# Kernel optimization log

Hardware: AMD Instinct MI355X
Metric: run time of the kernel (lower is better)

Reference implementation:

```python
import jax, jax.numpy as jnp
import numpy as np


def setup_inputs() -> dict:
    key = jax.random.key(0)
    k1, k2, k3, k4, k5 = jax.random.split(key, 5)
    B, S, H, F, E = 2, 512, 1024, 3584, 8
    scale_in = 1.0 / np.sqrt(H)
    scale_ff = 1.0 / np.sqrt(F)
    return {
        "hidden_states": jax.random.normal(k1, (B, S, H), dtype=jnp.float32),
        "gate_w": jax.random.normal(k2, (E, H), dtype=jnp.float32) * scale_in,
        "w1": jax.random.normal(k3, (E, F, H), dtype=jnp.float32) * scale_in,
        "w2": jax.random.normal(k4, (E, H, F), dtype=jnp.float32) * scale_ff,
        "w3": jax.random.normal(k5, (E, F, H), dtype=jnp.float32) * scale_in,
    }


TOP_K = 2


def reference(hidden_states, gate_w, w1, w2, w3):
    B, S, H = hidden_states.shape
    E = gate_w.shape[0]
    x = hidden_states.reshape(B * S, H)  # [T, H]
    T = x.shape[0]

    # Router: softmax in fp32, top-2 selection, renormalize selected weights.
    router_logits = x @ gate_w.T  # [T, E]
    probs = jax.nn.softmax(router_logits.astype(jnp.float32), axis=-1)
    top_vals, top_idx = jax.lax.top_k(probs, TOP_K)  # [T, K]
    top_vals = top_vals / jnp.sum(top_vals, axis=-1, keepdims=True)
    top_vals = top_vals.astype(x.dtype)

    # Dense routing-weight matrix [T, E]: weight if selected else 0
    # (equivalent to the one-hot expert_mask + index_add combine).
    dense_w = jnp.zeros((T, E), dtype=x.dtype).at[
        jnp.arange(T)[:, None], top_idx
    ].add(top_vals)

    # Expert SwiGLU MLPs, batched over the expert axis.
    h1 = jnp.einsum("th,efh->etf", x, w1)  # [E, T, F]
    h3 = jnp.einsum("th,efh->etf", x, w3)  # [E, T, F]
    y = jnp.einsum("etf,ehf->eth", jax.nn.silu(h1) * h3, w2)  # [E, T, H]

    # Weighted combine across experts.
    out = jnp.einsum("eth,te->th", y, dense_w)  # [T, H]
    return out.reshape(B, S, H), router_logits
```

## Files before the change

### kernel.cpp

```cpp
#include <hip/hip_runtime.h>
#include <hip/hip_bf16.h>

typedef __bf16 v8bf __attribute__((ext_vector_type(8)));
typedef __bf16 v4bf __attribute__((ext_vector_type(4)));
typedef float  f32x4 __attribute__((ext_vector_type(4)));
typedef unsigned int u32;

#define NTOK 1024
#define HDIM 1024
#define FDIM 3584
#define NEXP 8
#define NPAIR 2048
#define MAXT1 32
#define MAXT2 48
#define KSPLIT2 2
#define KPER2 (FDIM / KSPLIT2)

#define OFF_COUNTS   0
#define OFF_OFFSETS  64
#define OFF_NT1      128
#define OFF_NT2      132
#define OFF_T1E      192
#define OFF_T1M      320
#define OFF_T2E      448
#define OFF_T2M      640
#define OFF_TOKIDX   2048
#define OFF_TOKWT    (2048 + 4*NPAIR)
#define OFF_PAIRTOK  (OFF_TOKWT + 4*NPAIR)
#define OFF_PAIRWT   (OFF_PAIRTOK + 4*NPAIR)
#define OFF_SLOTOF   (OFF_PAIRWT + 4*NPAIR)
#define OFF_XB       65536
#define OFF_ACT      (OFF_XB + 2ull*NTOK*HDIM)
#define OFF_Y0       (OFF_ACT + 2ull*NPAIR*FDIM)
#define OFF_Y1       (OFF_Y0 + 4ull*NPAIR*HDIM)

static __device__ inline v4bf cvt4(float4 f) {
    v4bf r;
    r[0] = (__bf16)f.x; r[1] = (__bf16)f.y; r[2] = (__bf16)f.z; r[3] = (__bf16)f.w;
    return r;
}

static __device__ inline v8bf pack8(f32x4 lo, f32x4 hi) {
    v8bf r;
    r[0] = (__bf16)lo[0]; r[1] = (__bf16)lo[1]; r[2] = (__bf16)lo[2]; r[3] = (__bf16)lo[3];
    r[4] = (__bf16)hi[0]; r[5] = (__bf16)hi[1]; r[6] = (__bf16)hi[2]; r[7] = (__bf16)hi[3];
    return r;
}

#define FENCE() asm volatile("" ::: "memory")
#define BARRIER() do { FENCE(); __builtin_amdgcn_s_barrier(); FENCE(); } while (0)
#define WAITVM0() asm volatile("s_waitcnt vmcnt(0)" ::: "memory")
#define WAITLGKM0() asm volatile("s_waitcnt lgkmcnt(0)" ::: "memory")

#define DMA16(SRC, DST) \
    __builtin_amdgcn_global_load_lds((const __attribute__((address_space(1))) u32*)(SRC), \
                                     (__attribute__((address_space(3))) u32*)(DST), 16, 0, 0)

__global__ __launch_bounds__(256) void moe_cvtx(const float* __restrict__ x,
                                                __bf16* __restrict__ xb)
{
    const size_t i = ((size_t)blockIdx.x * 256 + threadIdx.x) * 4;
    float4 v = *(const float4*)(x + i);
    *(v4bf*)(xb + i) = cvt4(v);
}

__global__ __launch_bounds__(256) void moe_router(
    const float* __restrict__ x, const float* __restrict__ gw,
    float* __restrict__ logits, int* __restrict__ counts,
    int* __restrict__ tok_idx, float* __restrict__ tok_wt)
{
    const int lane = threadIdx.x & 63;
    const int wv = threadIdx.x >> 6;
    const int t = blockIdx.x * 4 + wv;
    const float* xr = x + (size_t)t * HDIM;

    float acc[NEXP];
#pragma unroll
    for (int e = 0; e < NEXP; ++e) acc[e] = 0.f;
#pragma unroll
    for (int j = 0; j < 4; ++j) {
        int h = lane * 4 + j * 256;
        float4 xv = *(const float4*)(xr + h);
#pragma unroll
        for (int e = 0; e < NEXP; ++e) {
            float4 g = *(const float4*)(gw + e * HDIM + h);
            acc[e] += xv.x * g.x + xv.y * g.y + xv.z * g.z + xv.w * g.w;
        }
    }
#pragma unroll
    for (int e = 0; e < NEXP; ++e) {
#pragma unroll
        for (int s = 32; s > 0; s >>= 1) acc[e] += __shfl_xor(acc[e], s);
    }
    if (lane == 0) {
#pragma unroll
        for (int e = 0; e < NEXP; ++e) logits[t * NEXP + e] = acc[e];
        int i0 = 0;
#pragma unroll
        for (int e = 1; e < NEXP; ++e) if (acc[e] > acc[i0]) i0 = e;
        int i1 = (i0 == 0) ? 1 : 0;
#pragma unroll
        for (int e = 0; e < NEXP; ++e) if (e != i0 && acc[e] > acc[i1]) i1 = e;
        float w0 = 1.f / (1.f + expf(acc[i1] - acc[i0]));
        float w1 = 1.f - w0;
        tok_idx[2 * t] = i0; tok_idx[2 * t + 1] = i1;
        tok_wt[2 * t] = w0;  tok_wt[2 * t + 1] = w1;
        atomicAdd(&counts[i0], 1);
        atomicAdd(&counts[i1], 1);
    }
}

__global__ void moe_scatter(const int* __restrict__ counts, const int* __restrict__ tok_idx,
                            const float* __restrict__ tok_wt, int* __restrict__ offsets,
                            int* __restrict__ pair_token, float* __restrict__ pair_wt,
                            int* __restrict__ slot_of,
                            int* __restrict__ t1e, int* __restrict__ t1m, int* __restrict__ nt1,
                            int* __restrict__ t2e, int* __restrict__ t2m, int* __restrict__ nt2)
{
    __shared__ int cur[NEXP];
    const int tid = threadIdx.x;
    if (tid == 0) {
        int run = 0, n1 = 0, n2 = 0;
        for (int e = 0; e < NEXP; ++e) {
            offsets[e] = run; cur[e] = run;
            for (int m0 = 0; m0 < counts[e]; m0 += 128) { t1e[n1] = e; t1m[n1] = m0; ++n1; }
            for (int m0 = 0; m0 < counts[e]; m0 += 64)  { t2e[n2] = e; t2m[n2] = m0; ++n2; }
            run += counts[e];
        }
        *nt1 = n1; *nt2 = n2;
    }
    __syncthreads();
    for (int p = tid; p < 2 * NTOK; p += blockDim.x) {
        int e = tok_idx[p];
        int s = atomicAdd(&cur[e], 1);
        pair_token[s] = p >> 1;
        pair_wt[s] = tok_wt[p];
        slot_of[p] = s;
    }
}

__global__ __launch_bounds__(256, 2) void moe_gemm1(
    const __bf16* __restrict__ xb, const float* __restrict__ w1g,
    const float* __restrict__ w3g, const int* __restrict__ counts,
    const int* __restrict__ offsets, const int* __restrict__ pair_token,
    const int* __restrict__ t1e, const int* __restrict__ t1m,
    const int* __restrict__ nt1,
    __bf16* __restrict__ act)
{
    const int ty = blockIdx.y;
    if (ty >= *nt1) return;
    const int e = t1e[ty];
    const int m0 = t1m[ty];
    const int Me = counts[e];
    const int rows = min(128, Me - m0);
    const int slot0 = offsets[e] + m0;
    const int n0 = blockIdx.x * 64;

    __shared__ __align__(16) __bf16 As[128 * 64];
    __shared__ __align__(16) float  B1s[64 * 64];
    __shared__ __align__(16) float  B3s[64 * 64];

    const int tid = threadIdx.x;
    const int lane = tid & 63;
    const int wv = tid >> 6;
    const int ln4 = lane >> 4;
    const int lr = lane & 15;
    const int wm = (wv >> 1) * 64;
    const int wn = (wv & 1) * 32;

    f32x4 acc1[4][2], acc3[4][2];
#pragma unroll
    for (int i = 0; i < 4; ++i)
#pragma unroll
        for (int j = 0; j < 2; ++j) {
            acc1[i][j] = (f32x4){0.f, 0.f, 0.f, 0.f};
            acc3[i][j] = (f32x4){0.f, 0.f, 0.f, 0.f};
        }

    const char* asrc[4];
#pragma unroll
    for (int i = 0; i < 4; ++i) {
        int c = i * 256 + tid;
        int r = c >> 3;
        int rr = (r < rows) ? r : 0;
        int sj = (c & 7) ^ (r & 7);
        asrc[i] = (const char*)(xb + (size_t)pair_token[slot0 + rr] * HDIM) + sj * 16;
    }
    const char* bsrc[4];
#pragma unroll
    for (int i = 0; i < 4; ++i) {
        int c = i * 256 + tid;
        int r = c >> 4;
        int sj = (c & 15) ^ (r & 15);
        bsrc[i] = (const char*)(w1g + ((size_t)e * FDIM + n0 + r) * HDIM) + sj * 16;
    }
    const ptrdiff_t d31b = (const char*)w3g - (const char*)w1g;

#define DMA_ALL1(K0) do { _Pragma("unroll") \
    for (int i = 0; i < 4; ++i) { \
        DMA16(asrc[i] + (size_t)(K0) * 128, (char*)As + (i * 256 + wv * 64) * 16); \
        DMA16(bsrc[i] + (size_t)(K0) * 256, (char*)B1s + (i * 256 + wv * 64) * 16); \
        DMA16(bsrc[i] + d31b + (size_t)(K0) * 256, (char*)B3s + (i * 256 + wv * 64) * 16); \
    } } while (0)

    int abase[4], axor[4];
#pragma unroll
    for (int i = 0; i < 4; ++i) {
        int row = wm + i * 16 + lr;
        abase[i] = row * 128;
        axor[i] = (row & 7) << 4;
    }
    int bbase[2], bxor[2];
#pragma unroll
    for (int i = 0; i < 2; ++i) {
        int row = wn + i * 16 + lr;
        bbase[i] = row * 256;
        bxor[i] = (row & 15) << 4;
    }

#define CMP1() do { \
    v8bf af[4][2]; v8bf b1f[2][2], b3f[2][2]; \
    _Pragma("unroll") \
    for (int mi = 0; mi < 4; ++mi) { _Pragma("unroll") \
        for (int ks = 0; ks < 2; ++ks) \
            af[mi][ks] = *(const v8bf*)((const char*)As + abase[mi] + ((ks * 64 + ln4 * 16) ^ axor[mi])); } \
    _Pragma("unroll") \
    for (int ni = 0; ni < 2; ++ni) { _Pragma("unroll") \
        for (int ks = 0; ks < 2; ++ks) { \
            int in0 = ks * 128 + ln4 * 32; \
            f32x4 lo1 = *(const f32x4*)((const char*)B1s + bbase[ni] + ((in0) ^ bxor[ni])); \
            f32x4 hi1 = *(const f32x4*)((const char*)B1s + bbase[ni] + ((in0 + 16) ^ bxor[ni])); \
            f32x4 lo3 = *(const f32x4*)((const char*)B3s + bbase[ni] + ((in0) ^ bxor[ni])); \
            f32x4 hi3 = *(const f32x4*)((const char*)B3s + bbase[ni] + ((in0 + 16) ^ bxor[ni])); \
            b1f[ni][ks] = pack8(lo1, hi1); \
            b3f[ni][ks] = pack8(lo3, hi3); } } \
    _Pragma("unroll") \
    for (int mi = 0; mi < 4; ++mi) { _Pragma("unroll") \
        for (int ni = 0; ni < 2; ++ni) { _Pragma("unroll") \
            for (int ks = 0; ks < 2; ++ks) { \
                acc1[mi][ni] = __builtin_amdgcn_mfma_f32_16x16x32_bf16(af[mi][ks], b1f[ni][ks], acc1[mi][ni], 0, 0, 0); \
                acc3[mi][ni] = __builtin_amdgcn_mfma_f32_16x16x32_bf16(af[mi][ks], b3f[ni][ks], acc3[mi][ni], 0, 0, 0); } } } \
    } while (0)

    DMA_ALL1(0);
    for (int ks = 0; ks < HDIM / 64; ++ks) {
        WAITVM0();
        BARRIER();
        CMP1();
        WAITLGKM0();
        BARRIER();
        if (ks + 1 < HDIM / 64) DMA_ALL1(ks + 1);
    }
#undef DMA_ALL1
#undef CMP1

    const int rj = ln4 * 4;
#pragma unroll
    for (int mi = 0; mi < 4; ++mi) {
#pragma unroll
        for (int j = 0; j < 4; ++j) {
            int rm = wm + mi * 16 + rj + j;
            if (rm < rows) {
                size_t rowoff = (size_t)(slot0 + rm) * FDIM + n0 + wn;
#pragma unroll
                for (int ni = 0; ni < 2; ++ni) {
                    float h1 = acc1[mi][ni][j];
                    float h3 = acc3[mi][ni][j];
                    float sv = (h1 / (1.f + __expf(-h1))) * h3;
                    act[rowoff + ni * 16 + lr] = (__bf16)sv;
                }
            }
        }
    }
}

__global__ __launch_bounds__(256, 2) void moe_gemm2(
    const __bf16* __restrict__ act, const float* __restrict__ w2g,
    const int* __restrict__ counts, const int* __restrict__ offsets,
    const int* __restrict__ t2e, const int* __restrict__ t2m,
    const int* __restrict__ nt2,
    float* __restrict__ y0, float* __restrict__ y1)
{
    const int ty = blockIdx.y;
    if (ty >= *nt2) return;
    const int e = t2e[ty];
    const int m0 = t2m[ty];
    const int Me = counts[e];
    const int rows = min(64, Me - m0);
    const int slot0 = offsets[e] + m0;
    const int n0 = blockIdx.x * 64;
    const int kz = blockIdx.z;
    float* yout = kz ? y1 : y0;
    const size_t kbase = (size_t)kz * KPER2;

    __shared__ __align__(16) __bf16 As[64 * 64];
    __shared__ __align__(16) float  Bs[64 * 64];

    const int tid = threadIdx.x;
    const int lane = tid & 63;
    const int wv = tid >> 6;
    const int ln4 = lane >> 4;
    const int lr = lane & 15;
    const int wm = (wv >> 1) * 32;
    const int wn = (wv & 1) * 32;

    f32x4 acc[2][2];
#pragma unroll
    for (int i = 0; i < 2; ++i)
#pragma unroll
        for (int j = 0; j < 2; ++j) acc[i][j] = (f32x4){0.f, 0.f, 0.f, 0.f};

    const char* asrc[2];
#pragma unroll
    for (int i = 0; i < 2; ++i) {
        int c = i * 256 + tid;
        int r = c >> 3;
        int rr = (r < rows) ? r : 0;
        int sj = (c & 7) ^ (r & 7);
        asrc[i] = (const char*)(act + (size_t)(slot0 + rr) * FDIM + kbase) + sj * 16;
    }
    const char* bsrc[4];
#pragma unroll
    for (int i = 0; i < 4; ++i) {
        int c = i * 256 + tid;
        int r = c >> 4;
        int sj = (c & 15) ^ (r & 15);
        bsrc[i] = (const char*)(w2g + ((size_t)e * HDIM + n0 + r) * FDIM + kbase) + sj * 16;
    }

#define DMA_ALL2(K0) do { \
    _Pragma("unroll") \
    for (int i = 0; i < 2; ++i) \
        DMA16(asrc[i] + (size_t)(K0) * 128, (char*)As + (i * 256 + wv * 64) * 16); \
    _Pragma("unroll") \
    for (int i = 0; i < 4; ++i) \
        DMA16(bsrc[i] + (size_t)(K0) * 256, (char*)Bs + (i * 256 + wv * 64) * 16); \
    } while (0)

    int abase[2], axor[2];
#pragma unroll
    for (int i = 0; i < 2; ++i) {
        int row = wm + i * 16 + lr;
        abase[i] = row * 128;
        axor[i] = (row & 7) << 4;
    }
    int bbase[2], bxor[2];
#pragma unroll
    for (int i = 0; i < 2; ++i) {
        int row = wn + i * 16 + lr;
        bbase[i] = row * 256;
        bxor[i] = (row & 15) << 4;
    }

#define CMP2() do { \
    v8bf af[2][2], bf[2][2]; \
    _Pragma("unroll") \
    for (int mi = 0; mi < 2; ++mi) { _Pragma("unroll") \
        for (int ks = 0; ks < 2; ++ks) \
            af[mi][ks] = *(const v8bf*)((const char*)As + abase[mi] + ((ks * 64 + ln4 * 16) ^ axor[mi])); } \
    _Pragma("unroll") \
    for (int ni = 0; ni < 2; ++ni) { _Pragma("unroll") \
        for (int ks = 0; ks < 2; ++ks) { \
            int in0 = ks * 128 + ln4 * 32; \
            f32x4 lo = *(const f32x4*)((const char*)Bs + bbase[ni] + ((in0) ^ bxor[ni])); \
            f32x4 hi = *(const f32x4*)((const char*)Bs + bbase[ni] + ((in0 + 16) ^ bxor[ni])); \
            bf[ni][ks] = pack8(lo, hi); } } \
    _Pragma("unroll") \
    for (int mi = 0; mi < 2; ++mi) { _Pragma("unroll") \
        for (int ni = 0; ni < 2; ++ni) { _Pragma("unroll") \
            for (int ks = 0; ks < 2; ++ks) \
                acc[mi][ni] = __builtin_amdgcn_mfma_f32_16x16x32_bf16(af[mi][ks], bf[ni][ks], acc[mi][ni], 0, 0, 0); } } \
    } while (0)

    DMA_ALL2(0);
    for (int ks = 0; ks < KPER2 / 64; ++ks) {
        WAITVM0();
        BARRIER();
        CMP2();
        WAITLGKM0();
        BARRIER();
        if (ks + 1 < KPER2 / 64) DMA_ALL2(ks + 1);
    }
#undef DMA_ALL2
#undef CMP2

    const int rj = ln4 * 4;
#pragma unroll
    for (int mi = 0; mi < 2; ++mi) {
#pragma unroll
        for (int j = 0; j < 4; ++j) {
            int rm = wm + mi * 16 + rj + j;
            if (rm < rows) {
                size_t rowoff = (size_t)(slot0 + rm) * HDIM + n0 + wn;
#pragma unroll
                for (int ni = 0; ni < 2; ++ni)
                    yout[rowoff + ni * 16 + lr] = acc[mi][ni][j];
            }
        }
    }
}

__global__ __launch_bounds__(256) void moe_combine(
    const float* __restrict__ y0, const float* __restrict__ y1,
    const int* __restrict__ slot_of, const float* __restrict__ pair_wt,
    float* __restrict__ out)
{
    const int t = blockIdx.x;
    const int tid = threadIdx.x;
    const int s0 = slot_of[2 * t];
    const int s1 = slot_of[2 * t + 1];
    const float w0 = pair_wt[s0];
    const float w1 = pair_wt[s1];
    const float4 a0 = *(const float4*)(y0 + (size_t)s0 * HDIM + tid * 4);
    const float4 a1 = *(const float4*)(y1 + (size_t)s0 * HDIM + tid * 4);
    const float4 b0 = *(const float4*)(y0 + (size_t)s1 * HDIM + tid * 4);
    const float4 b1 = *(const float4*)(y1 + (size_t)s1 * HDIM + tid * 4);
    float4 o;
    o.x = w0 * (a0.x + a1.x) + w1 * (b0.x + b1.x);
    o.y = w0 * (a0.y + a1.y) + w1 * (b0.y + b1.y);
    o.z = w0 * (a0.z + a1.z) + w1 * (b0.z + b1.z);
    o.w = w0 * (a0.w + a1.w) + w1 * (b0.w + b1.w);
    *(float4*)(out + (size_t)t * HDIM + tid * 4) = o;
}

extern "C" void kernel_launch(void* const* d_in, const int* in_sizes, int n_in,
                              void* d_out, int out_size, void* d_ws, size_t ws_size,
                              hipStream_t stream) {
    const float* x   = (const float*)d_in[0];
    const float* gw  = (const float*)d_in[1];
    const float* w1  = (const float*)d_in[2];
    const float* w2  = (const float*)d_in[3];
    const float* w3  = (const float*)d_in[4];

    float* out    = (float*)d_out;
    float* logits = out + (size_t)NTOK * HDIM;

    char* ws = (char*)d_ws;
    int*    counts     = (int*)(ws + OFF_COUNTS);
    int*    offsets    = (int*)(ws + OFF_OFFSETS);
    int*    nt1        = (int*)(ws + OFF_NT1);
    int*    nt2        = (int*)(ws + OFF_NT2);
    int*    t1e        = (int*)(ws + OFF_T1E);
    int*    t1m        = (int*)(ws + OFF_T1M);
    int*    t2e        = (int*)(ws + OFF_T2E);
    int*    t2m        = (int*)(ws + OFF_T2M);
    int*    tok_idx    = (int*)(ws + OFF_TOKIDX);
    float*  tok_wt     = (float*)(ws + OFF_TOKWT);
    int*    pair_token = (int*)(ws + OFF_PAIRTOK);
    float*  pair_wt    = (float*)(ws + OFF_PAIRWT);
    int*    slot_of    = (int*)(ws + OFF_SLOTOF);
    __bf16* xb         = (__bf16*)(ws + OFF_XB);
    __bf16* act        = (__bf16*)(ws + OFF_ACT);
    float*  yb0        = (float*)(ws + OFF_Y0);
    float*  yb1        = (float*)(ws + OFF_Y1);

    hipMemsetAsync(counts, 0, 64, stream);

    moe_cvtx<<<dim3(NTOK * HDIM / 1024), dim3(256), 0, stream>>>(x, xb);
    moe_router<<<dim3(NTOK / 4), dim3(256), 0, stream>>>(x, gw, logits, counts, tok_idx, tok_wt);
    moe_scatter<<<dim3(1), dim3(256), 0, stream>>>(counts, tok_idx, tok_wt, offsets,
                                                   pair_token, pair_wt, slot_of,
                                                   t1e, t1m, nt1, t2e, t2m, nt2);
    moe_gemm1<<<dim3(FDIM / 64, MAXT1), dim3(256), 0, stream>>>(
        xb, w1, w3, counts, offsets, pair_token, t1e, t1m, nt1, act);
    moe_gemm2<<<dim3(HDIM / 64, MAXT2, KSPLIT2), dim3(256), 0, stream>>>(
        act, w2, counts, offsets, t2e, t2m, nt2, yb0, yb1);
    moe_combine<<<dim3(NTOK), dim3(256), 0, stream>>>(yb0, yb1, slot_of, pair_wt, out);
}
```

Baseline: 196.3 us.

## Halve K-tile depth, enlarge gemm2 tiles to 128x128, raise split-K to four

Both GEMMs now use a 32-deep K tile, which halves shared-memory use so the launch bounds can request four blocks per CU instead of two. gemm2 moves from 64x64 tiles to 128x128 tiles, reuses the gemm1 128-row tile list, and splits K four ways into a single strided y buffer. The combine kernel sums the four partials. This trades more barriers per K step and more partial-sum traffic for higher occupancy and more operand reuse in gemm2.

```diff
diff --git a/kernel.cpp b/kernel.cpp
--- a/kernel.cpp
+++ b/kernel.cpp
@@ -11,19 +11,15 @@
 #define FDIM 3584
 #define NEXP 8
 #define NPAIR 2048
-#define MAXT1 32
-#define MAXT2 48
-#define KSPLIT2 2
+#define MAXT 32
+#define KSPLIT2 4
 #define KPER2 (FDIM / KSPLIT2)
 
 #define OFF_COUNTS   0
 #define OFF_OFFSETS  64
 #define OFF_NT1      128
-#define OFF_NT2      132
 #define OFF_T1E      192
 #define OFF_T1M      320
-#define OFF_T2E      448
-#define OFF_T2M      640
 #define OFF_TOKIDX   2048
 #define OFF_TOKWT    (2048 + 4*NPAIR)
 #define OFF_PAIRTOK  (OFF_TOKWT + 4*NPAIR)
@@ -31,8 +27,8 @@
 #define OFF_SLOTOF   (OFF_PAIRWT + 4*NPAIR)
 #define OFF_XB       65536
 #define OFF_ACT      (OFF_XB + 2ull*NTOK*HDIM)
-#define OFF_Y0       (OFF_ACT + 2ull*NPAIR*FDIM)
-#define OFF_Y1       (OFF_Y0 + 4ull*NPAIR*HDIM)
+#define OFF_Y        (OFF_ACT + 2ull*NPAIR*FDIM)
+#define YSTRIDE      ((size_t)NPAIR * HDIM)
 
 static __device__ inline v4bf cvt4(float4 f) {
     v4bf r;
@@ -114,20 +110,18 @@
                             const float* __restrict__ tok_wt, int* __restrict__ offsets,
                             int* __restrict__ pair_token, float* __restrict__ pair_wt,
                             int* __restrict__ slot_of,
-                            int* __restrict__ t1e, int* __restrict__ t1m, int* __restrict__ nt1,
-                            int* __restrict__ t2e, int* __restrict__ t2m, int* __restrict__ nt2)
+                            int* __restrict__ t1e, int* __restrict__ t1m, int* __restrict__ nt1)
 {
     __shared__ int cur[NEXP];
     const int tid = threadIdx.x;
     if (tid == 0) {
-        int run = 0, n1 = 0, n2 = 0;
+        int run = 0, n1 = 0;
         for (int e = 0; e < NEXP; ++e) {
             offsets[e] = run; cur[e] = run;
             for (int m0 = 0; m0 < counts[e]; m0 += 128) { t1e[n1] = e; t1m[n1] = m0; ++n1; }
-            for (int m0 = 0; m0 < counts[e]; m0 += 64)  { t2e[n2] = e; t2m[n2] = m0; ++n2; }
             run += counts[e];
         }
-        *nt1 = n1; *nt2 = n2;
+        *nt1 = n1;
     }
     __syncthreads();
     for (int p = tid; p < 2 * NTOK; p += blockDim.x) {
@@ -139,7 +133,7 @@
     }
 }
 
-__global__ __launch_bounds__(256, 2) void moe_gemm1(
+__global__ __launch_bounds__(256, 4) void moe_gemm1(
     const __bf16* __restrict__ xb, const float* __restrict__ w1g,
     const float* __restrict__ w3g, const int* __restrict__ counts,
     const int* __restrict__ offsets, const int* __restrict__ pair_token,
@@ -156,9 +150,9 @@
     const int slot0 = offsets[e] + m0;
     const int n0 = blockIdx.x * 64;
 
-    __shared__ __align__(16) __bf16 As[128 * 64];
-    __shared__ __align__(16) float  B1s[64 * 64];
-    __shared__ __align__(16) float  B3s[64 * 64];
+    __shared__ __align__(16) __bf16 As[128 * 32];
+    __shared__ __align__(16) float  B1s[64 * 32];
+    __shared__ __align__(16) float  B3s[64 * 32];
 
     const int tid = threadIdx.x;
     const int lane = tid & 63;
@@ -177,79 +171,71 @@
             acc3[i][j] = (f32x4){0.f, 0.f, 0.f, 0.f};
         }
 
-    const char* asrc[4];
-#pragma unroll
-    for (int i = 0; i < 4; ++i) {
+    const char* asrc[2];
+#pragma unroll
+    for (int i = 0; i < 2; ++i) {
+        int c = i * 256 + tid;
+        int r = c >> 2;
+        int rr = (r < rows) ? r : 0;
+        int sj = (c & 3) ^ ((r >> 1) & 3);
+        asrc[i] = (const char*)(xb + (size_t)pair_token[slot0 + rr] * HDIM) + sj * 16;
+    }
+    const char* bsrc[2];
+#pragma unroll
+    for (int i = 0; i < 2; ++i) {
         int c = i * 256 + tid;
         int r = c >> 3;
-        int rr = (r < rows) ? r : 0;
         int sj = (c & 7) ^ (r & 7);
-        asrc[i] = (const char*)(xb + (size_t)pair_token[slot0 + rr] * HDIM) + sj * 16;
-    }
-    const char* bsrc[4];
-#pragma unroll
-    for (int i = 0; i < 4; ++i) {
-        int c = i * 256 + tid;
-        int r = c >> 4;
-        int sj = (c & 15) ^ (r & 15);
         bsrc[i] = (const char*)(w1g + ((size_t)e * FDIM + n0 + r) * HDIM) + sj * 16;
     }
     const ptrdiff_t d31b = (const char*)w3g - (const char*)w1g;
 
 #define DMA_ALL1(K0) do { _Pragma("unroll") \
-    for (int i = 0; i < 4; ++i) { \
-        DMA16(asrc[i] + (size_t)(K0) * 128, (char*)As + (i * 256 + wv * 64) * 16); \
-        DMA16(bsrc[i] + (size_t)(K0) * 256, (char*)B1s + (i * 256 + wv * 64) * 16); \
-        DMA16(bsrc[i] + d31b + (size_t)(K0) * 256, (char*)B3s + (i * 256 + wv * 64) * 16); \
+    for (int i = 0; i < 2; ++i) { \
+        DMA16(asrc[i] + (size_t)(K0) * 64,         (char*)As  + (i * 256 + wv * 64) * 16); \
+        DMA16(bsrc[i] + (size_t)(K0) * 128,        (char*)B1s + (i * 256 + wv * 64) * 16); \
+        DMA16(bsrc[i] + d31b + (size_t)(K0) * 128, (char*)B3s + (i * 256 + wv * 64) * 16); \
     } } while (0)
 
-    int abase[4], axor[4];
+    int aoff[4];
 #pragma unroll
     for (int i = 0; i < 4; ++i) {
         int row = wm + i * 16 + lr;
-        abase[i] = row * 128;
-        axor[i] = (row & 7) << 4;
-    }
-    int bbase[2], bxor[2];
+        aoff[i] = row * 64 + ((ln4 ^ ((row >> 1) & 3)) * 16);
+    }
+    int blo[2], bhi[2];
 #pragma unroll
     for (int i = 0; i < 2; ++i) {
         int row = wn + i * 16 + lr;
-        bbase[i] = row * 256;
-        bxor[i] = (row & 15) << 4;
+        blo[i] = row * 128 + (((ln4 * 2) ^ (row & 7)) * 16);
+        bhi[i] = row * 128 + (((ln4 * 2 + 1) ^ (row & 7)) * 16);
     }
 
 #define CMP1() do { \
-    v8bf af[4][2]; v8bf b1f[2][2], b3f[2][2]; \
+    v8bf af[4], b1f[2], b3f[2]; \
+    _Pragma("unroll") \
+    for (int i = 0; i < 4; ++i) af[i] = *(const v8bf*)((const char*)As + aoff[i]); \
+    _Pragma("unroll") \
+    for (int i = 0; i < 2; ++i) { \
+        b1f[i] = pack8(*(const f32x4*)((const char*)B1s + blo[i]), \
+                       *(const f32x4*)((const char*)B1s + bhi[i])); \
+        b3f[i] = pack8(*(const f32x4*)((const char*)B3s + blo[i]), \
+                       *(const f32x4*)((const char*)B3s + bhi[i])); } \
     _Pragma("unroll") \
     for (int mi = 0; mi < 4; ++mi) { _Pragma("unroll") \
-        for (int ks = 0; ks < 2; ++ks) \
-            af[mi][ks] = *(const v8bf*)((const char*)As + abase[mi] + ((ks * 64 + ln4 * 16) ^ axor[mi])); } \
-    _Pragma("unroll") \
-    for (int ni = 0; ni < 2; ++ni) { _Pragma("unroll") \
-        for (int ks = 0; ks < 2; ++ks) { \
-            int in0 = ks * 128 + ln4 * 32; \
-            f32x4 lo1 = *(const f32x4*)((const char*)B1s + bbase[ni] + ((in0) ^ bxor[ni])); \
-            f32x4 hi1 = *(const f32x4*)((const char*)B1s + bbase[ni] + ((in0 + 16) ^ bxor[ni])); \
-            f32x4 lo3 = *(const f32x4*)((const char*)B3s + bbase[ni] + ((in0) ^ bxor[ni])); \
-            f32x4 hi3 = *(const f32x4*)((const char*)B3s + bbase[ni] + ((in0 + 16) ^ bxor[ni])); \
-            b1f[ni][ks] = pack8(lo1, hi1); \
-            b3f[ni][ks] = pack8(lo3, hi3); } } \
-    _Pragma("unroll") \
-    for (int mi = 0; mi < 4; ++mi) { _Pragma("unroll") \
-        for (int ni = 0; ni < 2; ++ni) { _Pragma("unroll") \
-            for (int ks = 0; ks < 2; ++ks) { \
-                acc1[mi][ni] = __builtin_amdgcn_mfma_f32_16x16x32_bf16(af[mi][ks], b1f[ni][ks], acc1[mi][ni], 0, 0, 0); \
-                acc3[mi][ni] = __builtin_amdgcn_mfma_f32_16x16x32_bf16(af[mi][ks], b3f[ni][ks], acc3[mi][ni], 0, 0, 0); } } } \
+        for (int ni = 0; ni < 2; ++ni) { \
+            acc1[mi][ni] = __builtin_amdgcn_mfma_f32_16x16x32_bf16(af[mi], b1f[ni], acc1[mi][ni], 0, 0, 0); \
+            acc3[mi][ni] = __builtin_amdgcn_mfma_f32_16x16x32_bf16(af[mi], b3f[ni], acc3[mi][ni], 0, 0, 0); } } \
     } while (0)
 
     DMA_ALL1(0);
-    for (int ks = 0; ks < HDIM / 64; ++ks) {
+    for (int ks = 0; ks < HDIM / 32; ++ks) {
         WAITVM0();
         BARRIER();
         CMP1();
         WAITLGKM0();
         BARRIER();
-        if (ks + 1 < HDIM / 64) DMA_ALL1(ks + 1);
+        if (ks + 1 < HDIM / 32) DMA_ALL1(ks + 1);
     }
 #undef DMA_ALL1
 #undef CMP1
@@ -274,126 +260,119 @@
     }
 }
 
-__global__ __launch_bounds__(256, 2) void moe_gemm2(
+__global__ __launch_bounds__(256, 4) void moe_gemm2(
     const __bf16* __restrict__ act, const float* __restrict__ w2g,
     const int* __restrict__ counts, const int* __restrict__ offsets,
-    const int* __restrict__ t2e, const int* __restrict__ t2m,
-    const int* __restrict__ nt2,
-    float* __restrict__ y0, float* __restrict__ y1)
+    const int* __restrict__ t1e, const int* __restrict__ t1m,
+    const int* __restrict__ nt1,
+    float* __restrict__ y)
 {
     const int ty = blockIdx.y;
-    if (ty >= *nt2) return;
-    const int e = t2e[ty];
-    const int m0 = t2m[ty];
+    if (ty >= *nt1) return;
+    const int e = t1e[ty];
+    const int m0 = t1m[ty];
     const int Me = counts[e];
-    const int rows = min(64, Me - m0);
+    const int rows = min(128, Me - m0);
     const int slot0 = offsets[e] + m0;
-    const int n0 = blockIdx.x * 64;
+    const int n0 = blockIdx.x * 128;
     const int kz = blockIdx.z;
-    float* yout = kz ? y1 : y0;
+    float* yout = y + (size_t)kz * YSTRIDE;
     const size_t kbase = (size_t)kz * KPER2;
 
-    __shared__ __align__(16) __bf16 As[64 * 64];
-    __shared__ __align__(16) float  Bs[64 * 64];
+    __shared__ __align__(16) __bf16 As[128 * 32];
+    __shared__ __align__(16) float  Bs[128 * 32];
 
     const int tid = threadIdx.x;
     const int lane = tid & 63;
     const int wv = tid >> 6;
     const int ln4 = lane >> 4;
     const int lr = lane & 15;
-    const int wm = (wv >> 1) * 32;
-    const int wn = (wv & 1) * 32;
-
-    f32x4 acc[2][2];
-#pragma unroll
-    for (int i = 0; i < 2; ++i)
-#pragma unroll
-        for (int j = 0; j < 2; ++j) acc[i][j] = (f32x4){0.f, 0.f, 0.f, 0.f};
+    const int wm = (wv >> 1) * 64;
+    const int wn = (wv & 1) * 64;
+
+    f32x4 acc[4][4];
+#pragma unroll
+    for (int i = 0; i < 4; ++i)
+#pragma unroll
+        for (int j = 0; j < 4; ++j) acc[i][j] = (f32x4){0.f, 0.f, 0.f, 0.f};
 
     const char* asrc[2];
 #pragma unroll
     for (int i = 0; i < 2; ++i) {
         int c = i * 256 + tid;
-        int r = c >> 3;
+        int r = c >> 2;
         int rr = (r < rows) ? r : 0;
-        int sj = (c & 7) ^ (r & 7);
+        int sj = (c & 3) ^ ((r >> 1) & 3);
         asrc[i] = (const char*)(act + (size_t)(slot0 + rr) * FDIM + kbase) + sj * 16;
     }
     const char* bsrc[4];
 #pragma unroll
     for (int i = 0; i < 4; ++i) {
         int c = i * 256 + tid;
-        int r = c >> 4;
-        int sj = (c & 15) ^ (r & 15);
+        int r = c >> 3;
+        int sj = (c & 7) ^ (r & 7);
         bsrc[i] = (const char*)(w2g + ((size_t)e * HDIM + n0 + r) * FDIM + kbase) + sj * 16;
     }
 
 #define DMA_ALL2(K0) do { \
     _Pragma("unroll") \
     for (int i = 0; i < 2; ++i) \
-        DMA16(asrc[i] + (size_t)(K0) * 128, (char*)As + (i * 256 + wv * 64) * 16); \
+        DMA16(asrc[i] + (size_t)(K0) * 64, (char*)As + (i * 256 + wv * 64) * 16); \
     _Pragma("unroll") \
     for (int i = 0; i < 4; ++i) \
-        DMA16(bsrc[i] + (size_t)(K0) * 256, (char*)Bs + (i * 256 + wv * 64) * 16); \
+        DMA16(bsrc[i] + (size_t)(K0) * 128, (char*)Bs + (i * 256 + wv * 64) * 16); \
     } while (0)
 
-    int abase[2], axor[2];
-#pragma unroll
-    for (int i = 0; i < 2; ++i) {
+    int aoff[4];
+#pragma unroll
+    for (int i = 0; i < 4; ++i) {
         int row = wm + i * 16 + lr;
-        abase[i] = row * 128;
-        axor[i] = (row & 7) << 4;
-    }
-    int bbase[2], bxor[2];
-#pragma unroll
-    for (int i = 0; i < 2; ++i) {
+        aoff[i] = row * 64 + ((ln4 ^ ((row >> 1) & 3)) * 16);
+    }
+    int blo[4], bhi[4];
+#pragma unroll
+    for (int i = 0; i < 4; ++i) {
         int row = wn + i * 16 + lr;
-        bbase[i] = row * 256;
-        bxor[i] = (row & 15) << 4;
+        blo[i] = row * 128 + (((ln4 * 2) ^ (row & 7)) * 16);
+        bhi[i] = row * 128 + (((ln4 * 2 + 1) ^ (row & 7)) * 16);
     }
 
 #define CMP2() do { \
-    v8bf af[2][2], bf[2][2]; \
-    _Pragma("unroll") \
-    for (int mi = 0; mi < 2; ++mi) { _Pragma("unroll") \
-        for (int ks = 0; ks < 2; ++ks) \
-            af[mi][ks] = *(const v8bf*)((const char*)As + abase[mi] + ((ks * 64 + ln4 * 16) ^ axor[mi])); } \
-    _Pragma("unroll") \
-    for (int ni = 0; ni < 2; ++ni) { _Pragma("unroll") \
-        for (int ks = 0; ks < 2; ++ks) { \
-            int in0 = ks * 128 + ln4 * 32; \
-            f32x4 lo = *(const f32x4*)((const char*)Bs + bbase[ni] + ((in0) ^ bxor[ni])); \
-            f32x4 hi = *(const f32x4*)((const char*)Bs + bbase[ni] + ((in0 + 16) ^ bxor[ni])); \
-            bf[ni][ks] = pack8(lo, hi); } } \
-    _Pragma("unroll") \
-    for (int mi = 0; mi < 2; ++mi) { _Pragma("unroll") \
-        for (int ni = 0; ni < 2; ++ni) { _Pragma("unroll") \
-            for (int ks = 0; ks < 2; ++ks) \
-                acc[mi][ni] = __builtin_amdgcn_mfma_f32_16x16x32_bf16(af[mi][ks], bf[ni][ks], acc[mi][ni], 0, 0, 0); } } \
+    v8bf af[4], bf[4]; \
+    _Pragma("unroll") \
+    for (int i = 0; i < 4; ++i) af[i] = *(const v8bf*)((const char*)As + aoff[i]); \
+    _Pragma("unroll") \
+    for (int i = 0; i < 4; ++i) \
+        bf[i] = pack8(*(const f32x4*)((const char*)Bs + blo[i]), \
+                      *(const f32x4*)((const char*)Bs + bhi[i])); \
+    _Pragma("unroll") \
+    for (int mi = 0; mi < 4; ++mi) { _Pragma("unroll") \
+        for (int ni = 0; ni < 4; ++ni) \
+            acc[mi][ni] = __builtin_amdgcn_mfma_f32_16x16x32_bf16(af[mi], bf[ni], acc[mi][ni], 0, 0, 0); } \
     } while (0)
 
     DMA_ALL2(0);
-    for (int ks = 0; ks < KPER2 / 64; ++ks) {
+    for (int ks = 0; ks < KPER2 / 32; ++ks) {
         WAITVM0();
         BARRIER();
         CMP2();
         WAITLGKM0();
         BARRIER();
-        if (ks + 1 < KPER2 / 64) DMA_ALL2(ks + 1);
+        if (ks + 1 < KPER2 / 32) DMA_ALL2(ks + 1);
     }
 #undef DMA_ALL2
 #undef CMP2
 
     const int rj = ln4 * 4;
 #pragma unroll
-    for (int mi = 0; mi < 2; ++mi) {
+    for (int mi = 0; mi < 4; ++mi) {
 #pragma unroll
         for (int j = 0; j < 4; ++j) {
             int rm = wm + mi * 16 + rj + j;
             if (rm < rows) {
                 size_t rowoff = (size_t)(slot0 + rm) * HDIM + n0 + wn;
 #pragma unroll
-                for (int ni = 0; ni < 2; ++ni)
+                for (int ni = 0; ni < 4; ++ni)
                     yout[rowoff + ni * 16 + lr] = acc[mi][ni][j];
             }
         }
@@ -401,9 +380,8 @@
 }
 
 __global__ __launch_bounds__(256) void moe_combine(
-    const float* __restrict__ y0, const float* __restrict__ y1,
-    const int* __restrict__ slot_of, const float* __restrict__ pair_wt,
-    float* __restrict__ out)
+    const float* __restrict__ y, const int* __restrict__ slot_of,
+    const float* __restrict__ pair_wt, float* __restrict__ out)
 {
     const int t = blockIdx.x;
     const int tid = threadIdx.x;
@@ -411,15 +389,19 @@
     const int s1 = slot_of[2 * t + 1];
     const float w0 = pair_wt[s0];
     const float w1 = pair_wt[s1];
-    const float4 a0 = *(const float4*)(y0 + (size_t)s0 * HDIM + tid * 4);
-    const float4 a1 = *(const float4*)(y1 + (size_t)s0 * HDIM + tid * 4);
-    const float4 b0 = *(const float4*)(y0 + (size_t)s1 * HDIM + tid * 4);
-    const float4 b1 = *(const float4*)(y1 + (size_t)s1 * HDIM + tid * 4);
+    float4 a = {0.f, 0.f, 0.f, 0.f}, b = {0.f, 0.f, 0.f, 0.f};
+#pragma unroll
+    for (int k = 0; k < KSPLIT2; ++k) {
+        const float4 ak = *(const float4*)(y + k * YSTRIDE + (size_t)s0 * HDIM + tid * 4);
+        const float4 bk = *(const float4*)(y + k * YSTRIDE + (size_t)s1 * HDIM + tid * 4);
+        a.x += ak.x; a.y += ak.y; a.z += ak.z; a.w += ak.w;
+        b.x += bk.x; b.y += bk.y; b.z += bk.z; b.w += bk.w;
+    }
     float4 o;
-    o.x = w0 * (a0.x + a1.x) + w1 * (b0.x + b1.x);
-    o.y = w0 * (a0.y + a1.y) + w1 * (b0.y + b1.y);
-    o.z = w0 * (a0.z + a1.z) + w1 * (b0.z + b1.z);
-    o.w = w0 * (a0.w + a1.w) + w1 * (b0.w + b1.w);
+    o.x = w0 * a.x + w1 * b.x;
+    o.y = w0 * a.y + w1 * b.y;
+    o.z = w0 * a.z + w1 * b.z;
+    o.w = w0 * a.w + w1 * b.w;
     *(float4*)(out + (size_t)t * HDIM + tid * 4) = o;
 }
 
@@ -439,11 +421,8 @@
     int*    counts     = (int*)(ws + OFF_COUNTS);
     int*    offsets    = (int*)(ws + OFF_OFFSETS);
     int*    nt1        = (int*)(ws + OFF_NT1);
-    int*    nt2        = (int*)(ws + OFF_NT2);
     int*    t1e        = (int*)(ws + OFF_T1E);
     int*    t1m        = (int*)(ws + OFF_T1M);
-    int*    t2e        = (int*)(ws + OFF_T2E);
-    int*    t2m        = (int*)(ws + OFF_T2M);
     int*    tok_idx    = (int*)(ws + OFF_TOKIDX);
     float*  tok_wt     = (float*)(ws + OFF_TOKWT);
     int*    pair_token = (int*)(ws + OFF_PAIRTOK);
@@ -451,8 +430,7 @@
     int*    slot_of    = (int*)(ws + OFF_SLOTOF);
     __bf16* xb         = (__bf16*)(ws + OFF_XB);
     __bf16* act        = (__bf16*)(ws + OFF_ACT);
-    float*  yb0        = (float*)(ws + OFF_Y0);
-    float*  yb1        = (float*)(ws + OFF_Y1);
+    float*  yb         = (float*)(ws + OFF_Y);
 
     hipMemsetAsync(counts, 0, 64, stream);
 
@@ -460,10 +438,10 @@
     moe_router<<<dim3(NTOK / 4), dim3(256), 0, stream>>>(x, gw, logits, counts, tok_idx, tok_wt);
     moe_scatter<<<dim3(1), dim3(256), 0, stream>>>(counts, tok_idx, tok_wt, offsets,
                                                    pair_token, pair_wt, slot_of,
-                                                   t1e, t1m, nt1, t2e, t2m, nt2);
-    moe_gemm1<<<dim3(FDIM / 64, MAXT1), dim3(256), 0, stream>>>(
+                                                   t1e, t1m, nt1);
+    moe_gemm1<<<dim3(FDIM / 64, MAXT), dim3(256), 0, stream>>>(
         xb, w1, w3, counts, offsets, pair_token, t1e, t1m, nt1, act);
-    moe_gemm2<<<dim3(HDIM / 64, MAXT2, KSPLIT2), dim3(256), 0, stream>>>(
-        act, w2, counts, offsets, t2e, t2m, nt2, yb0, yb1);
-    moe_combine<<<dim3(NTOK), dim3(256), 0, stream>>>(yb0, yb1, slot_of, pair_wt, out);
-}
+    moe_gemm2<<<dim3(HDIM / 128, MAXT, KSPLIT2), dim3(256), 0, stream>>>(
+        act, w2, counts, offsets, t1e, t1m, nt1, yb);
+    moe_combine<<<dim3(NTOK), dim3(256), 0, stream>>>(yb, slot_of, pair_wt, out);
+}
```

After: 220.4 us. 12.3% more time.

## Use 128-row M tiles and 4-way K split in MoE down-projection GEMM

Applied to the files above, without the earlier changes.

The second expert GEMM now uses 128-row token tiles, sharing the tile list with the first GEMM, so each w2 tile loaded into shared memory serves twice as many rows. The K split goes from 2 to 4 to keep enough blocks in flight, and the combine kernel sums four partial buffers. Launch-bounds occupancy hints are raised for both GEMMs. The trade-off is more register pressure, more fp32 partial-sum traffic through memory, and extra loads in the combine step.

```diff
diff --git a/kernel.cpp b/kernel.cpp
--- a/kernel.cpp
+++ b/kernel.cpp
@@ -11,19 +11,15 @@
 #define FDIM 3584
 #define NEXP 8
 #define NPAIR 2048
-#define MAXT1 32
-#define MAXT2 48
-#define KSPLIT2 2
+#define MAXT 32
+#define KSPLIT2 4
 #define KPER2 (FDIM / KSPLIT2)
 
 #define OFF_COUNTS   0
 #define OFF_OFFSETS  64
 #define OFF_NT1      128
-#define OFF_NT2      132
 #define OFF_T1E      192
 #define OFF_T1M      320
-#define OFF_T2E      448
-#define OFF_T2M      640
 #define OFF_TOKIDX   2048
 #define OFF_TOKWT    (2048 + 4*NPAIR)
 #define OFF_PAIRTOK  (OFF_TOKWT + 4*NPAIR)
@@ -31,8 +27,8 @@
 #define OFF_SLOTOF   (OFF_PAIRWT + 4*NPAIR)
 #define OFF_XB       65536
 #define OFF_ACT      (OFF_XB + 2ull*NTOK*HDIM)
-#define OFF_Y0       (OFF_ACT + 2ull*NPAIR*FDIM)
-#define OFF_Y1       (OFF_Y0 + 4ull*NPAIR*HDIM)
+#define OFF_Y        (OFF_ACT + 2ull*NPAIR*FDIM)
+#define YSTRIDE      ((size_t)NPAIR * HDIM)
 
 static __device__ inline v4bf cvt4(float4 f) {
     v4bf r;
@@ -114,20 +110,18 @@
                             const float* __restrict__ tok_wt, int* __restrict__ offsets,
                             int* __restrict__ pair_token, float* __restrict__ pair_wt,
                             int* __restrict__ slot_of,
-                            int* __restrict__ t1e, int* __restrict__ t1m, int* __restrict__ nt1,
-                            int* __restrict__ t2e, int* __restrict__ t2m, int* __restrict__ nt2)
+                            int* __restrict__ t1e, int* __restrict__ t1m, int* __restrict__ nt1)
 {
     __shared__ int cur[NEXP];
     const int tid = threadIdx.x;
     if (tid == 0) {
-        int run = 0, n1 = 0, n2 = 0;
+        int run = 0, n1 = 0;
         for (int e = 0; e < NEXP; ++e) {
             offsets[e] = run; cur[e] = run;
             for (int m0 = 0; m0 < counts[e]; m0 += 128) { t1e[n1] = e; t1m[n1] = m0; ++n1; }
-            for (int m0 = 0; m0 < counts[e]; m0 += 64)  { t2e[n2] = e; t2m[n2] = m0; ++n2; }
             run += counts[e];
         }
-        *nt1 = n1; *nt2 = n2;
+        *nt1 = n1;
     }
     __syncthreads();
     for (int p = tid; p < 2 * NTOK; p += blockDim.x) {
@@ -139,7 +133,7 @@
     }
 }
 
-__global__ __launch_bounds__(256, 2) void moe_gemm1(
+__global__ __launch_bounds__(256, 3) void moe_gemm1(
     const __bf16* __restrict__ xb, const float* __restrict__ w1g,
     const float* __restrict__ w3g, const int* __restrict__ counts,
     const int* __restrict__ offsets, const int* __restrict__ pair_token,
@@ -274,26 +268,26 @@
     }
 }
 
-__global__ __launch_bounds__(256, 2) void moe_gemm2(
+__global__ __launch_bounds__(256, 4) void moe_gemm2(
     const __bf16* __restrict__ act, const float* __restrict__ w2g,
     const int* __restrict__ counts, const int* __restrict__ offsets,
-    const int* __restrict__ t2e, const int* __restrict__ t2m,
-    const int* __restrict__ nt2,
-    float* __restrict__ y0, float* __restrict__ y1)
+    const int* __restrict__ t1e, const int* __restrict__ t1m,
+    const int* __restrict__ nt1,
+    float* __restrict__ y)
 {
     const int ty = blockIdx.y;
-    if (ty >= *nt2) return;
-    const int e = t2e[ty];
-    const int m0 = t2m[ty];
+    if (ty >= *nt1) return;
+    const int e = t1e[ty];
+    const int m0 = t1m[ty];
     const int Me = counts[e];
-    const int rows = min(64, Me - m0);
+    const int rows = min(128, Me - m0);
     const int slot0 = offsets[e] + m0;
     const int n0 = blockIdx.x * 64;
     const int kz = blockIdx.z;
-    float* yout = kz ? y1 : y0;
+    float* yout = y + (size_t)kz * YSTRIDE;
     const size_t kbase = (size_t)kz * KPER2;
 
-    __shared__ __align__(16) __bf16 As[64 * 64];
+    __shared__ __align__(16) __bf16 As[128 * 64];
     __shared__ __align__(16) float  Bs[64 * 64];
 
     const int tid = threadIdx.x;
@@ -301,18 +295,18 @@
     const int wv = tid >> 6;
     const int ln4 = lane >> 4;
     const int lr = lane & 15;
-    const int wm = (wv >> 1) * 32;
+    const int wm = (wv >> 1) * 64;
     const int wn = (wv & 1) * 32;
 
-    f32x4 acc[2][2];
-#pragma unroll
-    for (int i = 0; i < 2; ++i)
+    f32x4 acc[4][2];
+#pragma unroll
+    for (int i = 0; i < 4; ++i)
 #pragma unroll
         for (int j = 0; j < 2; ++j) acc[i][j] = (f32x4){0.f, 0.f, 0.f, 0.f};
 
-    const char* asrc[2];
-#pragma unroll
-    for (int i = 0; i < 2; ++i) {
+    const char* asrc[4];
+#pragma unroll
+    for (int i = 0; i < 4; ++i) {
         int c = i * 256 + tid;
         int r = c >> 3;
         int rr = (r < rows) ? r : 0;
@@ -328,18 +322,15 @@
         bsrc[i] = (const char*)(w2g + ((size_t)e * HDIM + n0 + r) * FDIM + kbase) + sj * 16;
     }
 
-#define DMA_ALL2(K0) do { \
-    _Pragma("unroll") \
-    for (int i = 0; i < 2; ++i) \
+#define DMA_ALL2(K0) do { _Pragma("unroll") \
+    for (int i = 0; i < 4; ++i) { \
         DMA16(asrc[i] + (size_t)(K0) * 128, (char*)As + (i * 256 + wv * 64) * 16); \
-    _Pragma("unroll") \
-    for (int i = 0; i < 4; ++i) \
         DMA16(bsrc[i] + (size_t)(K0) * 256, (char*)Bs + (i * 256 + wv * 64) * 16); \
-    } while (0)
-
-    int abase[2], axor[2];
-#pragma unroll
-    for (int i = 0; i < 2; ++i) {
+    } } while (0)
+
+    int abase[4], axor[4];
+#pragma unroll
+    for (int i = 0; i < 4; ++i) {
         int row = wm + i * 16 + lr;
         abase[i] = row * 128;
         axor[i] = (row & 7) << 4;
@@ -353,9 +344,9 @@
     }
 
 #define CMP2() do { \
-    v8bf af[2][2], bf[2][2]; \
-    _Pragma("unroll") \
-    for (int mi = 0; mi < 2; ++mi) { _Pragma("unroll") \
+    v8bf af[4][2], bf[2][2]; \
+    _Pragma("unroll") \
+    for (int mi = 0; mi < 4; ++mi) { _Pragma("unroll") \
         for (int ks = 0; ks < 2; ++ks) \
             af[mi][ks] = *(const v8bf*)((const char*)As + abase[mi] + ((ks * 64 + ln4 * 16) ^ axor[mi])); } \
     _Pragma("unroll") \
@@ -366,7 +357,7 @@
             f32x4 hi = *(const f32x4*)((const char*)Bs + bbase[ni] + ((in0 + 16) ^ bxor[ni])); \
             bf[ni][ks] = pack8(lo, hi); } } \
     _Pragma("unroll") \
-    for (int mi = 0; mi < 2; ++mi) { _Pragma("unroll") \
+    for (int mi = 0; mi < 4; ++mi) { _Pragma("unroll") \
         for (int ni = 0; ni < 2; ++ni) { _Pragma("unroll") \
             for (int ks = 0; ks < 2; ++ks) \
                 acc[mi][ni] = __builtin_amdgcn_mfma_f32_16x16x32_bf16(af[mi][ks], bf[ni][ks], acc[mi][ni], 0, 0, 0); } } \
@@ -386,7 +377,7 @@
 
     const int rj = ln4 * 4;
 #pragma unroll
-    for (int mi = 0; mi < 2; ++mi) {
+    for (int mi = 0; mi < 4; ++mi) {
 #pragma unroll
         for (int j = 0; j < 4; ++j) {
             int rm = wm + mi * 16 + rj + j;
@@ -401,9 +392,8 @@
 }
 
 __global__ __launch_bounds__(256) void moe_combine(
-    const float* __restrict__ y0, const float* __restrict__ y1,
-    const int* __restrict__ slot_of, const float* __restrict__ pair_wt,
-    float* __restrict__ out)
+    const float* __restrict__ y, const int* __restrict__ slot_of,
+    const float* __restrict__ pair_wt, float* __restrict__ out)
 {
     const int t = blockIdx.x;
     const int tid = threadIdx.x;
@@ -411,15 +401,19 @@
     const int s1 = slot_of[2 * t + 1];
     const float w0 = pair_wt[s0];
     const float w1 = pair_wt[s1];
-    const float4 a0 = *(const float4*)(y0 + (size_t)s0 * HDIM + tid * 4);
-    const float4 a1 = *(const float4*)(y1 + (size_t)s0 * HDIM + tid * 4);
-    const float4 b0 = *(const float4*)(y0 + (size_t)s1 * HDIM + tid * 4);
-    const float4 b1 = *(const float4*)(y1 + (size_t)s1 * HDIM + tid * 4);
+    float4 a = {0.f, 0.f, 0.f, 0.f}, b = {0.f, 0.f, 0.f, 0.f};
+#pragma unroll
+    for (int k = 0; k < KSPLIT2; ++k) {
+        const float4 ak = *(const float4*)(y + k * YSTRIDE + (size_t)s0 * HDIM + tid * 4);
+        const float4 bk = *(const float4*)(y + k * YSTRIDE + (size_t)s1 * HDIM + tid * 4);
+        a.x += ak.x; a.y += ak.y; a.z += ak.z; a.w += ak.w;
+        b.x += bk.x; b.y += bk.y; b.z += bk.z; b.w += bk.w;
+    }
     float4 o;
-    o.x = w0 * (a0.x + a1.x) + w1 * (b0.x + b1.x);
-    o.y = w0 * (a0.y + a1.y) + w1 * (b0.y + b1.y);
-    o.z = w0 * (a0.z + a1.z) + w1 * (b0.z + b1.z);
-    o.w = w0 * (a0.w + a1.w) + w1 * (b0.w + b1.w);
+    o.x = w0 * a.x + w1 * b.x;
+    o.y = w0 * a.y + w1 * b.y;
+    o.z = w0 * a.z + w1 * b.z;
+    o.w = w0 * a.w + w1 * b.w;
     *(float4*)(out + (size_t)t * HDIM + tid * 4) = o;
 }
 
@@ -439,11 +433,8 @@
     int*    counts     = (int*)(ws + OFF_COUNTS);
     int*    offsets    = (int*)(ws + OFF_OFFSETS);
     int*    nt1        = (int*)(ws + OFF_NT1);
-    int*    nt2        = (int*)(ws + OFF_NT2);
     int*    t1e        = (int*)(ws + OFF_T1E);
     int*    t1m        = (int*)(ws + OFF_T1M);
-    int*    t2e        = (int*)(ws + OFF_T2E);
-    int*    t2m        = (int*)(ws + OFF_T2M);
     int*    tok_idx    = (int*)(ws + OFF_TOKIDX);
     float*  tok_wt     = (float*)(ws + OFF_TOKWT);
     int*    pair_token = (int*)(ws + OFF_PAIRTOK);
@@ -451,8 +442,7 @@
     int*    slot_of    = (int*)(ws + OFF_SLOTOF);
     __bf16* xb         = (__bf16*)(ws + OFF_XB);
     __bf16* act        = (__bf16*)(ws + OFF_ACT);
-    float*  yb0        = (float*)(ws + OFF_Y0);
-    float*  yb1        = (float*)(ws + OFF_Y1);
+    float*  yb         = (float*)(ws + OFF_Y);
 
     hipMemsetAsync(counts, 0, 64, stream);
 
@@ -460,10 +450,10 @@
     moe_router<<<dim3(NTOK / 4), dim3(256), 0, stream>>>(x, gw, logits, counts, tok_idx, tok_wt);
     moe_scatter<<<dim3(1), dim3(256), 0, stream>>>(counts, tok_idx, tok_wt, offsets,
                                                    pair_token, pair_wt, slot_of,
-                                                   t1e, t1m, nt1, t2e, t2m, nt2);
-    moe_gemm1<<<dim3(FDIM / 64, MAXT1), dim3(256), 0, stream>>>(
+                                                   t1e, t1m, nt1);
+    moe_gemm1<<<dim3(FDIM / 64, MAXT), dim3(256), 0, stream>>>(
         xb, w1, w3, counts, offsets, pair_token, t1e, t1m, nt1, act);
-    moe_gemm2<<<dim3(HDIM / 64, MAXT2, KSPLIT2), dim3(256), 0, stream>>>(
-        act, w2, counts, offsets, t2e, t2m, nt2, yb0, yb1);
-    moe_combine<<<dim3(NTOK), dim3(256), 0, stream>>>(yb0, yb1, slot_of, pair_wt, out);
-}
+    moe_gemm2<<<dim3(HDIM / 64, MAXT, KSPLIT2), dim3(256), 0, stream>>>(
+        act, w2, counts, offsets, t1e, t1m, nt1, yb);
+    moe_combine<<<dim3(NTOK), dim3(256), 0, stream>>>(yb, slot_of, pair_wt, out);
+}
```

New measurement: 193.0 us. No clear change (-1.7%).
